# Performance work log

Hardware: AMD Instinct MI355X
Metric: run time of the kernel (lower is better)

Reference implementation:

```python
import jax, jax.numpy as jnp
import numpy as np

B, N, T_OBS, N_HEAD = 64, 512, 8, 4
IN_FEAT = T_OBS * 2          # 16
OUT_FEAT = IN_FEAT * 4       # 64 (GAT out / MLP in)
HID1, HID2 = 1024, 512
S, NSAMP = 2, 20
OUT_DIM = S * NSAMP          # 40


def setup_inputs() -> dict:
    key = jax.random.key(0)
    ks = jax.random.split(key, 12)
    x = jax.random.normal(ks[0], (B, N, T_OBS, 2), dtype=jnp.float32)
    # binary adjacency-style mask over the dense node-node attention
    mask = (jax.random.uniform(ks[1], (B, 1, N, N)) > 0.1).astype(jnp.float32)
    xav = lambda k, shp, fi, fo: jax.random.uniform(k, shp, jnp.float32, -1.0, 1.0) * (1.414 * np.sqrt(6.0 / (fi + fo)))
    w = xav(ks[2], (N_HEAD, IN_FEAT, OUT_FEAT), IN_FEAT, OUT_FEAT)
    a_src = xav(ks[3], (N_HEAD, OUT_FEAT, 1), OUT_FEAT, 1)
    a_dst = xav(ks[4], (N_HEAD, OUT_FEAT, 1), OUT_FEAT, 1)
    bias = jnp.zeros((OUT_FEAT,), jnp.float32)
    lin = lambda k, fi, fo: jax.random.uniform(k, (fi, fo), jnp.float32, -1.0, 1.0) * np.sqrt(1.0 / fi)
    W1 = lin(ks[5], OUT_FEAT, HID1); b1 = jnp.zeros((HID1,), jnp.float32)
    W2 = lin(ks[6], HID1, HID2);     b2 = jnp.zeros((HID2,), jnp.float32)
    W3 = lin(ks[7], HID2, OUT_DIM);  b3 = jnp.zeros((OUT_DIM,), jnp.float32)
    return {"x": x, "mask": mask, "w": w, "a_src": a_src, "a_dst": a_dst,
            "bias": bias, "W1": W1, "b1": b1, "W2": W2, "b2": b2, "W3": W3, "b3": b3}


def reference(x, mask, w, a_src, a_dst, bias, W1, b1, W2, b2, W3, b3):
    b, n = x.shape[0], x.shape[1]
    node = x.reshape(b, n, -1)                                   # [B,N,16]
    # per-head projection: [B,N,16] x [H,16,64] -> [B,H,N,64]
    h_prime = jnp.einsum('bni,hio->bhno', node, w)
    attn_src = jnp.einsum('bhno,ho->bhn', h_prime, a_src[..., 0])
    attn_dst = jnp.einsum('bhno,ho->bhn', h_prime, a_dst[..., 0])
    attn = attn_src[..., :, None] * attn_dst[..., None, :]       # [B,H,N,N] outer product
    attn = jnp.where(attn >= 0, attn, 0.2 * attn)                # leaky_relu(0.2)
    attn = jax.nn.softmax(attn, axis=-1)
    # dropout is identity in eval mode
    attn = attn * mask
    out = jnp.einsum('bhnm,bhmo->bno', attn, h_prime) + bias     # sum over heads fused
    out = out + h_prime.sum(axis=1)                              # skip connection
    # MLP: activation BEFORE each linear (as in original MLP.forward)
    y = out
    for W, bb in ((W1, b1), (W2, b2), (W3, b3)):
        y = jax.nn.relu(y) @ W + bb
    y = y.reshape(b, n, NSAMP, -1)[..., 0:S]                     # [B,N,20,2]
    return jnp.clip(jax.nn.sigmoid(y), 0.01, 0.99)
```

## Files before the change

### kernel.cpp

```cpp
#include <hip/hip_runtime.h>
#include <math.h>

typedef short bf16x8 __attribute__((ext_vector_type(8)));
typedef float f32x4 __attribute__((ext_vector_type(4)));

#define BB 64
#define NN 512
#define NH 4
#define FI 16
#define FO 64
#define HD1 1024
#define HD2 512
#define ODIM 40

__device__ __forceinline__ unsigned short f2bf(float f) {
    unsigned u = __float_as_uint(f);
    u += 0x7fffu + ((u >> 16) & 1u);
    return (unsigned short)(u >> 16);
}
__device__ __forceinline__ unsigned pack2(float a, float b) {
    return (unsigned)f2bf(a) | ((unsigned)f2bf(b) << 16);
}
__device__ __forceinline__ void gload16(const void* g, void* l) {
    __builtin_amdgcn_global_load_lds(
        (const __attribute__((address_space(1))) unsigned int*)g,
        (__attribute__((address_space(3))) unsigned int*)l,
        16, 0, 0);
}

__global__ void k_wa(const float* __restrict__ w, const float* __restrict__ a_src,
                     const float* __restrict__ a_dst, float* __restrict__ wa)
{
    int t = threadIdx.x;
    int h = t >> 4;
    float s = 0.f, d = 0.f;
    for (int o = 0; o < FO; ++o) {
        float wv = w[t*FO + o];
        s = fmaf(wv, a_src[h*FO + o], s);
        d = fmaf(wv, a_dst[h*FO + o], d);
    }
    wa[t] = s; wa[64 + t] = d;
}

__global__ __launch_bounds__(256) void k_proj2(
    const float* __restrict__ x, const float* __restrict__ w,
    const float* __restrict__ bias, const float* __restrict__ wa,
    short* __restrict__ hpT,
    float* __restrict__ asrc, float* __restrict__ adst,
    float* __restrict__ gat)
{
    __shared__ float xS[64][20];
    __shared__ float gS[NH][64][64];
    int b = blockIdx.y;
    int n0 = blockIdx.x * 64;
    int t = threadIdx.x;
    int h = t >> 6, o = t & 63;
    {
        int n = t >> 2, q = t & 3;
        float4 v = *(const float4*)&x[((size_t)b*NN + n0 + n)*FI + q*4];
        *(float4*)&xS[n][q*4] = v;
    }
    float wreg[16];
#pragma unroll
    for (int i = 0; i < FI; ++i) wreg[i] = w[(h*FI + i)*FO + o];
    __syncthreads();

    short* hb = hpT + (size_t)b * (NH*FO*NN);
    for (int nc = 0; nc < 8; ++nc) {
        float acc[8];
#pragma unroll
        for (int k = 0; k < 8; ++k) {
            int n = nc*8 + k;
            float4 a0 = *(const float4*)&xS[n][0];
            float4 a1 = *(const float4*)&xS[n][4];
            float4 a2 = *(const float4*)&xS[n][8];
            float4 a3 = *(const float4*)&xS[n][12];
            float sA = fmaf(a0.x, wreg[0], fmaf(a0.y, wreg[1], fmaf(a0.z, wreg[2], a0.w*wreg[3])));
            float sB = fmaf(a1.x, wreg[4], fmaf(a1.y, wreg[5], fmaf(a1.z, wreg[6], a1.w*wreg[7])));
            float sC = fmaf(a2.x, wreg[8], fmaf(a2.y, wreg[9], fmaf(a2.z, wreg[10], a2.w*wreg[11])));
            float sD = fmaf(a3.x, wreg[12], fmaf(a3.y, wreg[13], fmaf(a3.z, wreg[14], a3.w*wreg[15])));
            float s = (sA + sB) + (sC + sD);
            acc[k] = s;
            gS[h][n][o] = s;
        }
        uint4 p;
        p.x = pack2(acc[0], acc[1]); p.y = pack2(acc[2], acc[3]);
        p.z = pack2(acc[4], acc[5]); p.w = pack2(acc[6], acc[7]);
        int jt = (n0 >> 5) + (nc >> 2);
        *(uint4*)&hb[(size_t)(jt*256 + h*64 + o)*32 + (nc & 3)*8] = p;
    }
    {
        int n = o;
        float vs = 0.f, vd = 0.f;
#pragma unroll
        for (int i = 0; i < FI; ++i) {
            float xv = xS[n][i];
            vs = fmaf(xv, wa[h*FI + i], vs);
            vd = fmaf(xv, wa[64 + h*FI + i], vd);
        }
        asrc[(size_t)(b*NH + h)*NN + n0 + n] = vs;
        adst[(size_t)(b*NH + h)*NN + n0 + n] = vd;
    }
    __syncthreads();
#pragma unroll
    for (int r = 0; r < 16; ++r) {
        int idx = t + r*256;
        int n = idx >> 6, oo = idx & 63;
        float g = bias[oo] + ((gS[0][n][oo] + gS[1][n][oo]) + (gS[2][n][oo] + gS[3][n][oo]));
        gat[((size_t)b*NN + n0 + n)*FO + oo] = g;
    }
}

__global__ __launch_bounds__(512, 2) void k_attn2(
    const short* __restrict__ hpT, const float* __restrict__ mask,
    const float* __restrict__ asrc, const float* __restrict__ adst,
    float* __restrict__ gat)
{
    __shared__ float dS[NH*NN];
    __shared__ float dmaxS[NH], dminS[NH];
    __shared__ float part[4*4*64*4];
    int b = blockIdx.y;
    int i0blk = blockIdx.x * 64;
    int t = threadIdx.x;
#pragma unroll
    for (int r = 0; r < 4; ++r) {
        int idx = t + r*512;
        dS[idx] = adst[(size_t)b*(NH*NN) + idx];
    }
    __syncthreads();
    int wave = t >> 6, lane = t & 63;
    int wv4 = wave & 3, hh = (wave >> 2) * 2;
    if (wave < 4) {
        float mx = -INFINITY, mn = INFINITY;
        const float* dh = &dS[wave*NN];
#pragma unroll
        for (int q = 0; q < 8; ++q) {
            float v = dh[lane*8 + q];
            mx = fmaxf(mx, v); mn = fminf(mn, v);
        }
#pragma unroll
        for (int off = 1; off < 64; off <<= 1) {
            mx = fmaxf(mx, __shfl_xor(mx, off));
            mn = fminf(mn, __shfl_xor(mn, off));
        }
        if (lane == 0) { dmaxS[wave] = mx; dminS[wave] = mn; }
    }
    __syncthreads();
    int li = lane & 15, kq = lane >> 4;
    int i = i0blk + wv4*16 + li;
    float s[2], m[2], Ssum[2];
#pragma unroll
    for (int h2 = 0; h2 < 2; ++h2) {
        int h = hh + h2;
        s[h2] = asrc[(size_t)(b*NH + h)*NN + i];
        float dm = s[h2] >= 0.f ? dmaxS[h] : dminS[h];
        float l = s[h2] * dm;
        m[h2] = fmaxf(l, 0.2f*l);
        Ssum[h2] = 0.f;
    }
    f32x4 accH[2][4];
#pragma unroll
    for (int h2 = 0; h2 < 2; ++h2)
#pragma unroll
        for (int ot = 0; ot < 4; ++ot) accH[h2][ot] = (f32x4)0.f;

    const float* mrow = &mask[((size_t)b*NN + i)*NN];
    const short* vb = hpT + (size_t)b * (NH*FO*NN);
    float4 mk0 = *(const float4*)&mrow[kq*8];
    float4 mk1 = *(const float4*)&mrow[kq*8 + 4];
    for (int jt = 0; jt < 16; ++jt) {
        float4 c0 = mk0, c1 = mk1;
        if (jt < 15) {
            mk0 = *(const float4*)&mrow[(jt+1)*32 + kq*8];
            mk1 = *(const float4*)&mrow[(jt+1)*32 + kq*8 + 4];
        }
        int j0 = jt*32;
        float mk[8] = {c0.x, c0.y, c0.z, c0.w, c1.x, c1.y, c1.z, c1.w};
#pragma unroll
        for (int h2 = 0; h2 < 2; ++h2) {
            int h = hh + h2;
            float4 d0 = *(const float4*)&dS[h*NN + j0 + kq*8];
            float4 d1 = *(const float4*)&dS[h*NN + j0 + kq*8 + 4];
            float dv[8] = {d0.x,d0.y,d0.z,d0.w,d1.x,d1.y,d1.z,d1.w};
            float u[8];
#pragma unroll
            for (int q = 0; q < 8; ++q) {
                float v = s[h2]*dv[q];
                v = fmaxf(v, 0.2f*v);
                u[q] = __expf(v - m[h2]);
            }
            Ssum[h2] += ((u[0]+u[1]) + (u[2]+u[3])) + ((u[4]+u[5]) + (u[6]+u[7]));
            union { bf16x8 v; unsigned uu[4]; } pf;
#pragma unroll
            for (int q = 0; q < 4; ++q)
                pf.uu[q] = pack2(u[2*q]*mk[2*q], u[2*q+1]*mk[2*q+1]);
#pragma unroll
            for (int ot = 0; ot < 4; ++ot) {
                bf16x8 vf = *(const bf16x8*)&vb[(size_t)(jt*256 + h*64 + ot*16 + li)*32 + kq*8];
                accH[h2][ot] = __builtin_amdgcn_mfma_f32_16x16x32_bf16(pf.v, vf, accH[h2][ot], 0, 0, 0);
            }
        }
    }
#pragma unroll
    for (int h2 = 0; h2 < 2; ++h2) {
        Ssum[h2] += __shfl_xor(Ssum[h2], 16);
        Ssum[h2] += __shfl_xor(Ssum[h2], 32);
    }
    float rinv[2][4];
#pragma unroll
    for (int h2 = 0; h2 < 2; ++h2)
#pragma unroll
        for (int g = 0; g < 4; ++g)
            rinv[h2][g] = 1.0f / __shfl(Ssum[h2], kq*4 + g);
    f32x4 contrib[4];
#pragma unroll
    for (int ot = 0; ot < 4; ++ot)
#pragma unroll
        for (int g = 0; g < 4; ++g)
            contrib[ot][g] = accH[0][ot][g]*rinv[0][g] + accH[1][ot][g]*rinv[1][g];
    if (wave < 4) {
#pragma unroll
        for (int ot = 0; ot < 4; ++ot) {
            float4 v = {contrib[ot][0], contrib[ot][1], contrib[ot][2], contrib[ot][3]};
            *(float4*)&part[((wv4*4 + ot)*64 + lane)*4] = v;
        }
    }
    __syncthreads();
    if (wave >= 4) {
#pragma unroll
        for (int ot = 0; ot < 4; ++ot) {
            float4 p = *(const float4*)&part[((wv4*4 + ot)*64 + lane)*4];
#pragma unroll
            for (int g = 0; g < 4; ++g) {
                int ii = i0blk + wv4*16 + kq*4 + g;
                int oo = ot*16 + li;
                size_t ix = ((size_t)b*NN + ii)*FO + oo;
                float pg = (g == 0) ? p.x : (g == 1) ? p.y : (g == 2) ? p.z : p.w;
                gat[ix] += contrib[ot][g] + pg;
            }
        }
    }
}

__global__ __launch_bounds__(256) void k_conv(
    const float* __restrict__ W1, const float* __restrict__ W2, const float* __restrict__ W3,
    short* __restrict__ w1t, short* __restrict__ w2f, short* __restrict__ w3t)
{
    int idx = blockIdx.x * 256 + threadIdx.x;
    if (idx < HD1*FO) {
        int n = idx >> 6, k = idx & 63;
        w1t[idx] = (short)f2bf(W1[k*HD1 + n]);
    } else if (idx < HD1*FO + HD2*HD1) {
        int i2 = idx - HD1*FO;
        int e = i2 & 7, kqq = (i2 >> 3) & 3, n = (i2 >> 5) & 511, ks = i2 >> 14;
        int k = ks*32 + kqq*8 + e;
        w2f[i2] = (short)f2bf(W2[k*HD2 + n]);
    } else if (idx < HD1*FO + HD2*HD1 + 48*HD2) {
        int i3 = idx - (HD1*FO + HD2*HD1);
        int n = i3 >> 9, k = i3 & 511;
        w3t[i3] = (short)(n < ODIM ? f2bf(W3[k*ODIM + n]) : 0);
    }
}

__global__ __launch_bounds__(256, 2) void k_mlpA(
    const float* __restrict__ gat,
    const short* __restrict__ w1t, const float* __restrict__ b1,
    short* __restrict__ h1g)
{
    __shared__ char a0b[8192];
    int t = threadIdx.x;
    int lane = t & 63, wave = t >> 6;
    int li = lane & 15, kq = lane >> 4;
    int m0 = blockIdx.x * 64;

    {
        int row = t >> 2, c0 = (t & 3) * 16;
        const float4* g = (const float4*)&gat[(size_t)(m0 + row) * FO + c0];
        float4 v0 = g[0], v1 = g[1], v2 = g[2], v3 = g[3];
        uint4 p0, p1;
        p0.x = pack2(fmaxf(v0.x,0.f), fmaxf(v0.y,0.f));
        p0.y = pack2(fmaxf(v0.z,0.f), fmaxf(v0.w,0.f));
        p0.z = pack2(fmaxf(v1.x,0.f), fmaxf(v1.y,0.f));
        p0.w = pack2(fmaxf(v1.z,0.f), fmaxf(v1.w,0.f));
        p1.x = pack2(fmaxf(v2.x,0.f), fmaxf(v2.y,0.f));
        p1.y = pack2(fmaxf(v2.z,0.f), fmaxf(v2.w,0.f));
        p1.z = pack2(fmaxf(v3.x,0.f), fmaxf(v3.y,0.f));
        p1.w = pack2(fmaxf(v3.z,0.f), fmaxf(v3.w,0.f));
        int base = row*128 + c0*2;
        *(uint4*)(a0b + (base ^ ((row&7)<<4)))      = p0;
        *(uint4*)(a0b + ((base+16) ^ ((row&7)<<4))) = p1;
    }
    __syncthreads();

    for (int c = 0; c < 4; ++c) {
        int n0 = wave * 256 + c * 64;
        f32x4 acc[4][4];
#pragma unroll
        for (int mt = 0; mt < 4; ++mt)
#pragma unroll
            for (int nt = 0; nt < 4; ++nt) acc[mt][nt] = (f32x4)0.f;
#pragma unroll
        for (int ks = 0; ks < 2; ++ks) {
            int k0 = ks * 32;
            bf16x8 xf[4];
#pragma unroll
            for (int mt = 0; mt < 4; ++mt) {
                int row = mt * 16 + li;
                int addr = (row * 128 + k0 * 2 + kq * 16) ^ ((row & 7) << 4);
                xf[mt] = *(bf16x8*)(a0b + addr);
            }
#pragma unroll
            for (int nt = 0; nt < 4; ++nt) {
                int col = n0 + nt * 16 + li;
                bf16x8 wf = *(const bf16x8*)(w1t + col * 64 + k0 + kq * 8);
#pragma unroll
                for (int mt = 0; mt < 4; ++mt)
                    acc[mt][nt] = __builtin_amdgcn_mfma_f32_16x16x32_bf16(wf, xf[mt], acc[mt][nt], 0, 0, 0);
            }
        }
#pragma unroll
        for (int mt = 0; mt < 4; ++mt)
#pragma unroll
            for (int nt = 0; nt < 4; ++nt) {
                int m = mt * 16 + li;
                int nb = n0 + nt * 16 + kq * 4;
                float4 bb = *(const float4*)&b1[nb];
                float v0 = fmaxf(acc[mt][nt][0] + bb.x, 0.f);
                float v1 = fmaxf(acc[mt][nt][1] + bb.y, 0.f);
                float v2 = fmaxf(acc[mt][nt][2] + bb.z, 0.f);
                float v3 = fmaxf(acc[mt][nt][3] + bb.w, 0.f);
                uint2 pw; pw.x = pack2(v0, v1); pw.y = pack2(v2, v3);
                *(uint2*)&h1g[(size_t)(m0 + m) * HD1 + nb] = pw;
            }
    }
}

__global__ __launch_bounds__(512, 2) void k_mlpB(
    const short* __restrict__ h1g,
    const short* __restrict__ w2f, const float* __restrict__ b2,
    const short* __restrict__ w3t, const float* __restrict__ b3,
    float* __restrict__ out)
{
    extern __shared__ char smem[];
    int t = threadIdx.x;
    int lane = t & 63, wave = t >> 6;
    int li = lane & 15, kq = lane >> 4;
    int m0 = blockIdx.x * 128;

    auto STAGE = [&](int i, int ks) {
        char* base = smem + i * 8192;
        int row = wave * 16 + (lane >> 2);
        int slotS = (lane & 3) ^ ((row >> 1) & 3);
        const short* src = h1g + (size_t)(m0 + row) * HD1 + ks * 32 + slotS * 8;
        gload16(src, base + wave * 1024);
    };
    const short* wfbase = w2f + ((size_t)(wave*64 + li)*4 + kq)*8;

    f32x4 acc2[8][4];
#pragma unroll
    for (int mt = 0; mt < 8; ++mt)
#pragma unroll
        for (int nt = 0; nt < 4; ++nt) acc2[mt][nt] = (f32x4)0.f;

    bf16x8 wf0[4], wf1[4];
    __builtin_amdgcn_sched_barrier(0);
    STAGE(0, 0);
#pragma unroll
    for (int nt = 0; nt < 4; ++nt) wf0[nt] = *(const bf16x8*)(wfbase + 0*16384 + nt*512);
    __builtin_amdgcn_sched_barrier(0);
    STAGE(1, 1);
#pragma unroll
    for (int nt = 0; nt < 4; ++nt) wf1[nt] = *(const bf16x8*)(wfbase + 1*16384 + nt*512);
    __builtin_amdgcn_sched_barrier(0);

    for (int ks = 0; ks < 32; ++ks) {
        int cur = ks & 1;
        if (ks < 31) { asm volatile("s_waitcnt vmcnt(5)" ::: "memory"); }
        else         { asm volatile("s_waitcnt vmcnt(0)" ::: "memory"); }
        __builtin_amdgcn_sched_barrier(0);
        __builtin_amdgcn_s_barrier();
        __builtin_amdgcn_sched_barrier(0);

        char* base = smem + cur * 8192;
        bf16x8 xf[8];
#pragma unroll
        for (int mt = 0; mt < 8; ++mt) {
            int m = mt * 16 + li;
            int slot = kq ^ ((m >> 1) & 3);
            xf[mt] = *(bf16x8*)(base + m * 64 + slot * 16);
        }
        asm volatile("s_waitcnt lgkmcnt(0)" ::: "memory");
        __builtin_amdgcn_sched_barrier(0);
        __builtin_amdgcn_s_barrier();
        __builtin_amdgcn_sched_barrier(0);

        bf16x8 wfn[4];
        if (ks < 30) {
            STAGE(cur, ks + 2);
#pragma unroll
            for (int nt = 0; nt < 4; ++nt)
                wfn[nt] = *(const bf16x8*)(wfbase + (size_t)(ks+2)*16384 + nt*512);
        }
        __builtin_amdgcn_sched_barrier(0);

#pragma unroll
        for (int nt = 0; nt < 4; ++nt)
#pragma unroll
            for (int mt = 0; mt < 8; ++mt)
                acc2[mt][nt] = __builtin_amdgcn_mfma_f32_16x16x32_bf16(wf0[nt], xf[mt], acc2[mt][nt], 0, 0, 0);
        if (ks < 30) {
#pragma unroll
            for (int nt = 0; nt < 4; ++nt) { wf0[nt] = wf1[nt]; wf1[nt] = wfn[nt]; }
        } else {
#pragma unroll
            for (int nt = 0; nt < 4; ++nt) wf0[nt] = wf1[nt];
        }
    }
    __syncthreads();

#pragma unroll
    for (int mt = 0; mt < 8; ++mt)
#pragma unroll
        for (int nt = 0; nt < 4; ++nt) {
            int m = mt * 16 + li;
            int nb = wave * 64 + nt * 16 + kq * 4;
            float4 bb = *(const float4*)&b2[nb];
            float v0 = fmaxf(acc2[mt][nt][0] + bb.x, 0.f);
            float v1 = fmaxf(acc2[mt][nt][1] + bb.y, 0.f);
            float v2 = fmaxf(acc2[mt][nt][2] + bb.z, 0.f);
            float v3 = fmaxf(acc2[mt][nt][3] + bb.w, 0.f);
            uint2 pw; pw.x = pack2(v0, v1); pw.y = pack2(v2, v3);
            int addr = (m * 1024 + nb * 2) ^ ((m & 7) << 4);
            *(uint2*)(smem + addr) = pw;
        }
    __syncthreads();

    f32x4 acc3[3];
#pragma unroll
    for (int nt = 0; nt < 3; ++nt) acc3[nt] = (f32x4)0.f;
#pragma unroll
    for (int ks = 0; ks < 16; ++ks) {
        int k0 = ks * 32;
        int m = wave * 16 + li;
        int addr = (m * 1024 + k0 * 2 + kq * 16) ^ ((m & 7) << 4);
        bf16x8 xf = *(bf16x8*)(smem + addr);
#pragma unroll
        for (int nt = 0; nt < 3; ++nt) {
            int col = nt * 16 + li;
            bf16x8 wf = *(const bf16x8*)(w3t + col * 512 + k0 + kq * 8);
            acc3[nt] = __builtin_amdgcn_mfma_f32_16x16x32_bf16(wf, xf, acc3[nt], 0, 0, 0);
        }
    }
#pragma unroll
    for (int nt = 0; nt < 3; ++nt)
#pragma unroll
        for (int g = 0; g < 4; ++g) {
            int n = nt * 16 + kq * 4 + g;
            if (n < ODIM) {
                int m = wave * 16 + li;
                float s = acc3[nt][g] + b3[n];
                s = 1.f / (1.f + __expf(-s));
                s = fminf(fmaxf(s, 0.01f), 0.99f);
                out[(size_t)(m0 + m) * ODIM + n] = s;
            }
        }
}

extern "C" void kernel_launch(void* const* d_in, const int* in_sizes, int n_in,
                              void* d_out, int out_size, void* d_ws, size_t ws_size,
                              hipStream_t stream)
{
    const float* x     = (const float*)d_in[0];
    const float* mask  = (const float*)d_in[1];
    const float* w     = (const float*)d_in[2];
    const float* a_src = (const float*)d_in[3];
    const float* a_dst = (const float*)d_in[4];
    const float* bias  = (const float*)d_in[5];
    const float* W1    = (const float*)d_in[6];
    const float* b1    = (const float*)d_in[7];
    const float* W2    = (const float*)d_in[8];
    const float* b2    = (const float*)d_in[9];
    const float* W3    = (const float*)d_in[10];
    const float* b3    = (const float*)d_in[11];
    float* out = (float*)d_out;

    char* p = (char*)d_ws;
    short* h1g = (short*)p;
    short* hpT = (short*)p;  p += (size_t)BB*NH*FO*NN*2;
    float* asrc = (float*)p; p += (size_t)BB*NH*NN*4;
    float* adst = (float*)p; p += (size_t)BB*NH*NN*4;
    p = (char*)d_ws + (size_t)BB*NN*HD1*2;
    float* gat  = (float*)p; p += (size_t)BB*NN*FO*4;
    short* w1t  = (short*)p; p += (size_t)HD1*FO*2;
    short* w2f  = (short*)p; p += (size_t)HD2*HD1*2;
    short* w3t  = (short*)p; p += (size_t)48*HD2*2;
    float* wa   = (float*)p; p += 128*4;

    k_wa   <<<1, 64, 0, stream>>>(w, a_src, a_dst, wa);
    k_conv <<<(HD1*FO + HD2*HD1 + 48*HD2)/256, 256, 0, stream>>>(W1, W2, W3, w1t, w2f, w3t);
    k_proj2<<<dim3(NN/64, BB), 256, 0, stream>>>(x, w, bias, wa, hpT, asrc, adst, gat);
    k_attn2<<<dim3(NN/64, BB), 512, 0, stream>>>(hpT, mask, asrc, adst, gat);
    k_mlpA <<<BB*NN/64, 256, 0, stream>>>(gat, w1t, b1, h1g);
    k_mlpB <<<BB*NN/128, 512, 131072, stream>>>(h1g, w2f, b2, w3t, b3, out);
}
```

Measured before the change: 160.9 us.

## Store MLP hidden activations in MFMA fragment layout and load directly to registers

k_mlpA now writes the first hidden layer in a k-slab-major layout that matches the MFMA operand fragment order. k_mlpB then reads its activation fragments straight from global memory into double-buffered registers. This removes the LDS staging, the swizzle and the two barriers per k-step from the second layer's GEMM. In exchange, every wave reloads the same activation fragments from global/L2 (eight waves share each row block), which raises global traffic and register pressure.

```diff
diff --git a/kernel.cpp b/kernel.cpp
--- a/kernel.cpp
+++ b/kernel.cpp
@@ -20,12 +20,6 @@
 }
 __device__ __forceinline__ unsigned pack2(float a, float b) {
     return (unsigned)f2bf(a) | ((unsigned)f2bf(b) << 16);
-}
-__device__ __forceinline__ void gload16(const void* g, void* l) {
-    __builtin_amdgcn_global_load_lds(
-        (const __attribute__((address_space(1))) unsigned int*)g,
-        (__attribute__((address_space(3))) unsigned int*)l,
-        16, 0, 0);
 }
 
 __global__ void k_wa(const float* __restrict__ w, const float* __restrict__ a_src,
@@ -265,7 +259,7 @@
 __global__ __launch_bounds__(256, 2) void k_mlpA(
     const float* __restrict__ gat,
     const short* __restrict__ w1t, const float* __restrict__ b1,
-    short* __restrict__ h1g)
+    short* __restrict__ h1f)
 {
     __shared__ char a0b[8192];
     int t = threadIdx.x;
@@ -330,13 +324,17 @@
                 float v2 = fmaxf(acc[mt][nt][2] + bb.z, 0.f);
                 float v3 = fmaxf(acc[mt][nt][3] + bb.w, 0.f);
                 uint2 pw; pw.x = pack2(v0, v1); pw.y = pack2(v2, v3);
-                *(uint2*)&h1g[(size_t)(m0 + m) * HD1 + nb] = pw;
+                int ks2 = wave*8 + c*2 + (nt >> 1);
+                int kq2 = ((nt*2) + (kq >> 1)) & 3;
+                int e0  = (kq & 1) * 4;
+                size_t dst = (size_t)ks2*1048576 + (size_t)(m0 + m)*32 + kq2*8 + e0;
+                *(uint2*)&h1f[dst] = pw;
             }
     }
 }
 
 __global__ __launch_bounds__(512, 2) void k_mlpB(
-    const short* __restrict__ h1g,
+    const short* __restrict__ h1f,
     const short* __restrict__ w2f, const float* __restrict__ b2,
     const short* __restrict__ w3t, const float* __restrict__ b3,
     float* __restrict__ out)
@@ -347,14 +345,8 @@
     int li = lane & 15, kq = lane >> 4;
     int m0 = blockIdx.x * 128;
 
-    auto STAGE = [&](int i, int ks) {
-        char* base = smem + i * 8192;
-        int row = wave * 16 + (lane >> 2);
-        int slotS = (lane & 3) ^ ((row >> 1) & 3);
-        const short* src = h1g + (size_t)(m0 + row) * HD1 + ks * 32 + slotS * 8;
-        gload16(src, base + wave * 1024);
-    };
-    const short* wfbase = w2f + ((size_t)(wave*64 + li)*4 + kq)*8;
+    const short* xbase = h1f + (size_t)(m0 + li) * 32 + kq * 8;
+    const short* wbase = w2f + ((size_t)(wave*64 + li)*4 + kq)*8;
 
     f32x4 acc2[8][4];
 #pragma unroll
@@ -362,61 +354,29 @@
 #pragma unroll
         for (int nt = 0; nt < 4; ++nt) acc2[mt][nt] = (f32x4)0.f;
 
-    bf16x8 wf0[4], wf1[4];
-    __builtin_amdgcn_sched_barrier(0);
-    STAGE(0, 0);
-#pragma unroll
-    for (int nt = 0; nt < 4; ++nt) wf0[nt] = *(const bf16x8*)(wfbase + 0*16384 + nt*512);
-    __builtin_amdgcn_sched_barrier(0);
-    STAGE(1, 1);
-#pragma unroll
-    for (int nt = 0; nt < 4; ++nt) wf1[nt] = *(const bf16x8*)(wfbase + 1*16384 + nt*512);
-    __builtin_amdgcn_sched_barrier(0);
-
+    bf16x8 xf[2][8], wf[2][4];
+#define LOADI(P, KS) do { \
+    _Pragma("unroll") \
+    for (int mt_ = 0; mt_ < 8; ++mt_) \
+        xf[P][mt_] = *(const bf16x8*)(xbase + (size_t)(KS)*1048576 + mt_*512); \
+    _Pragma("unroll") \
+    for (int nt_ = 0; nt_ < 4; ++nt_) \
+        wf[P][nt_] = *(const bf16x8*)(wbase + (size_t)(KS)*16384 + nt_*512); \
+} while (0)
+
+    LOADI(0, 0);
+    LOADI(1, 1);
+#pragma unroll 2
     for (int ks = 0; ks < 32; ++ks) {
-        int cur = ks & 1;
-        if (ks < 31) { asm volatile("s_waitcnt vmcnt(5)" ::: "memory"); }
-        else         { asm volatile("s_waitcnt vmcnt(0)" ::: "memory"); }
-        __builtin_amdgcn_sched_barrier(0);
-        __builtin_amdgcn_s_barrier();
-        __builtin_amdgcn_sched_barrier(0);
-
-        char* base = smem + cur * 8192;
-        bf16x8 xf[8];
-#pragma unroll
-        for (int mt = 0; mt < 8; ++mt) {
-            int m = mt * 16 + li;
-            int slot = kq ^ ((m >> 1) & 3);
-            xf[mt] = *(bf16x8*)(base + m * 64 + slot * 16);
-        }
-        asm volatile("s_waitcnt lgkmcnt(0)" ::: "memory");
-        __builtin_amdgcn_sched_barrier(0);
-        __builtin_amdgcn_s_barrier();
-        __builtin_amdgcn_sched_barrier(0);
-
-        bf16x8 wfn[4];
-        if (ks < 30) {
-            STAGE(cur, ks + 2);
-#pragma unroll
-            for (int nt = 0; nt < 4; ++nt)
-                wfn[nt] = *(const bf16x8*)(wfbase + (size_t)(ks+2)*16384 + nt*512);
-        }
-        __builtin_amdgcn_sched_barrier(0);
-
+        int p = ks & 1;
 #pragma unroll
         for (int nt = 0; nt < 4; ++nt)
 #pragma unroll
             for (int mt = 0; mt < 8; ++mt)
-                acc2[mt][nt] = __builtin_amdgcn_mfma_f32_16x16x32_bf16(wf0[nt], xf[mt], acc2[mt][nt], 0, 0, 0);
-        if (ks < 30) {
-#pragma unroll
-            for (int nt = 0; nt < 4; ++nt) { wf0[nt] = wf1[nt]; wf1[nt] = wfn[nt]; }
-        } else {
-#pragma unroll
-            for (int nt = 0; nt < 4; ++nt) wf0[nt] = wf1[nt];
-        }
-    }
-    __syncthreads();
+                acc2[mt][nt] = __builtin_amdgcn_mfma_f32_16x16x32_bf16(wf[p][nt], xf[p][mt], acc2[mt][nt], 0, 0, 0);
+        if (ks < 30) LOADI(p, ks + 2);
+    }
+#undef LOADI
 
 #pragma unroll
     for (int mt = 0; mt < 8; ++mt)
@@ -443,12 +403,12 @@
         int k0 = ks * 32;
         int m = wave * 16 + li;
         int addr = (m * 1024 + k0 * 2 + kq * 16) ^ ((m & 7) << 4);
-        bf16x8 xf = *(bf16x8*)(smem + addr);
+        bf16x8 xfr = *(bf16x8*)(smem + addr);
 #pragma unroll
         for (int nt = 0; nt < 3; ++nt) {
             int col = nt * 16 + li;
-            bf16x8 wf = *(const bf16x8*)(w3t + col * 512 + k0 + kq * 8);
-            acc3[nt] = __builtin_amdgcn_mfma_f32_16x16x32_bf16(wf, xf, acc3[nt], 0, 0, 0);
+            bf16x8 wfr = *(const bf16x8*)(w3t + col * 512 + k0 + kq * 8);
+            acc3[nt] = __builtin_amdgcn_mfma_f32_16x16x32_bf16(wfr, xfr, acc3[nt], 0, 0, 0);
         }
     }
 #pragma unroll
@@ -485,7 +445,7 @@
     float* out = (float*)d_out;
 
     char* p = (char*)d_ws;
-    short* h1g = (short*)p;
+    short* h1f = (short*)p;
     short* hpT = (short*)p;  p += (size_t)BB*NH*FO*NN*2;
     float* asrc = (float*)p; p += (size_t)BB*NH*NN*4;
     float* adst = (float*)p; p += (size_t)BB*NH*NN*4;
@@ -500,6 +460,6 @@
     k_conv <<<(HD1*FO + HD2*HD1 + 48*HD2)/256, 256, 0, stream>>>(W1, W2, W3, w1t, w2f, w3t);
     k_proj2<<<dim3(NN/64, BB), 256, 0, stream>>>(x, w, bias, wa, hpT, asrc, adst, gat);
     k_attn2<<<dim3(NN/64, BB), 512, 0, stream>>>(hpT, mask, asrc, adst, gat);
-    k_mlpA <<<BB*NN/64, 256, 0, stream>>>(gat, w1t, b1, h1g);
-    k_mlpB <<<BB*NN/128, 512, 131072, stream>>>(h1g, w2f, b2, w3t, b3, out);
-}
+    k_mlpA <<<BB*NN/64, 256, 0, stream>>>(gat, w1t, b1, h1f);
+    k_mlpB <<<BB*NN/128, 512, 131072, stream>>>(h1f, w2f, b2, w3t, b3, out);
+}
```

After: 167.4 us. 1.04x slower.
